# Performance work log

Measured on AMD Instinct MI355X. Metric: run time of the kernel, lower is better.

## Reference

```python
import jax, jax.numpy as jnp
import numpy as np

B, S, D, H = 4, 2048, 1024, 16
DK = D // H
NEG = -1e9


def setup_inputs() -> dict:
    key = jax.random.key(0)
    ks = jax.random.split(key, 8)
    q = jax.random.normal(ks[0], (B, S, D), dtype=jnp.float32)
    k = jax.random.normal(ks[1], (B, S, D), dtype=jnp.float32)
    v = jax.random.normal(ks[2], (B, S, D), dtype=jnp.float32)
    # causal mask, broadcastable to [B,H,S,S]; mask==0 -> masked out
    mask = jnp.tril(jnp.ones((S, S), dtype=jnp.int32))[None, None, :, :]
    scale = 1.0 / np.sqrt(D)
    w_q = jax.random.normal(ks[3], (D, D), dtype=jnp.float32) * scale
    w_k = jax.random.normal(ks[4], (D, D), dtype=jnp.float32) * scale
    w_v = jax.random.normal(ks[5], (D, D), dtype=jnp.float32) * scale
    w_o = jax.random.normal(ks[6], (D, D), dtype=jnp.float32) * scale
    return {"q": q, "k": k, "v": v, "mask": mask,
            "w_q": w_q, "w_k": w_k, "w_v": w_v, "w_o": w_o}


def reference(q, k, v, mask, w_q, w_k, w_v, w_o):
    # projections (nn.Linear with no bias: x @ W^T)
    def proj(x, w):
        y = jnp.einsum('bsd,ed->bse', x, w)          # [B,S,D]
        return y.reshape(B, -1, H, DK).transpose(0, 2, 1, 3)  # [B,H,S,DK]
    Q, K, V = proj(q, w_q), proj(k, w_k), proj(v, w_v)
    scores = jnp.einsum('bhqd,bhkd->bhqk', Q, K) * (DK ** -0.5)  # [B,H,S,S]
    scores = jnp.where(mask == 0, NEG, scores)
    attn = jax.nn.softmax(scores, axis=-1)
    x = jnp.einsum('bhqk,bhkd->bhqd', attn, V)       # [B,H,S,DK]
    x = x.transpose(0, 2, 1, 3).reshape(B, -1, D)    # [B,S,D]
    return jnp.einsum('bsd,ed->bse', x, w_o)
```

## Files before the change

### kernel.cpp

```cpp
#include <hip/hip_runtime.h>
#include <hip/hip_bf16.h>
#include <stdint.h>

#define B_ 4
#define S_ 2048
#define D_ 1024
#define H_ 16
#define DK_ 64

typedef __hip_bfloat16 bf16;
typedef __attribute__((ext_vector_type(8))) __bf16 bf16x8;
typedef __attribute__((ext_vector_type(4))) __bf16 bf16x4;
typedef __attribute__((ext_vector_type(4))) float f32x4;
typedef __attribute__((ext_vector_type(4))) uint32_t u32x4;

#define QSCALE 0.18033688011112042f

#if defined(__has_builtin)
#if __has_builtin(__builtin_amdgcn_exp2f)
#define EXP2(x) __builtin_amdgcn_exp2f(x)
#endif
#endif
#ifndef EXP2
#define EXP2(x) exp2f(x)
#endif

__device__ __forceinline__ void async_copy16(const void* g, void* l) {
    __builtin_amdgcn_global_load_lds((const __attribute__((address_space(1))) void*)g,
                                     (__attribute__((address_space(3))) void*)l,
                                     16, 0, 0);
}

__device__ __forceinline__ bf16x8 ld8(const bf16* p) {
    return *(const bf16x8*)p;
}

__device__ __forceinline__ uint32_t pk2(float a, float b) {
    union { __bf16 h; uint16_t u; } x, y;
    x.h = (__bf16)a; y.h = (__bf16)b;
    return (uint32_t)x.u | ((uint32_t)y.u << 16);
}

__device__ __forceinline__ bf16x8 cvt8(float4 u0, float4 u1) {
    return (bf16x8){(__bf16)u0.x, (__bf16)u0.y, (__bf16)u0.z, (__bf16)u0.w,
                    (__bf16)u1.x, (__bf16)u1.y, (__bf16)u1.z, (__bf16)u1.w};
}

__device__ __forceinline__ bf16x8 transpose_p(const float* p0, const float* p1,
                                              int srcl, bool loT) {
    uint32_t x0 = pk2(p0[0], p0[1]), x1 = pk2(p0[2], p0[3]);
    uint32_t y0 = pk2(p1[0], p1[1]), y1 = pk2(p1[2], p1[3]);
    u32x4 dw;
#pragma unroll
    for (int i = 0; i < 4; i++) {
        int sl = srcl + (i >> 1) * 16;
        uint32_t vA = (uint32_t)__shfl((int)((i & 1) ? x1 : x0), sl, 64);
        uint32_t vB = (uint32_t)__shfl((int)((i & 1) ? y1 : y0), sl, 64);
        dw[i] = loT ? vA : vB;
    }
    return __builtin_bit_cast(bf16x8, dw);
}

__global__ __launch_bounds__(256) void cvtw(const float4* __restrict__ s0,
                                            const float4* __restrict__ s1,
                                            const float4* __restrict__ s2,
                                            const float4* __restrict__ s3,
                                            bf16x4* __restrict__ d0,
                                            bf16x4* __restrict__ d1,
                                            bf16x4* __restrict__ d2,
                                            bf16x4* __restrict__ d3) {
    int i = blockIdx.x * 256 + threadIdx.x;
    int seg = i >> 18;
    int j   = i & 262143;
    const float4* s = seg == 0 ? s0 : seg == 1 ? s1 : seg == 2 ? s2 : s3;
    bf16x4*       d = seg == 0 ? d0 : seg == 1 ? d1 : seg == 2 ? d2 : d3;
    float4 f = s[j];
    d[j] = (bf16x4){(__bf16)f.x, (__bf16)f.y, (__bf16)f.z, (__bf16)f.w};
}

__global__ __launch_bounds__(256) void cvtx(const float* __restrict__ s0,
                                            const float* __restrict__ s1,
                                            const float* __restrict__ s2,
                                            bf16* __restrict__ d0,
                                            bf16* __restrict__ d1,
                                            bf16* __restrict__ d2) {
    const int z = blockIdx.z;
    const float* s = z == 0 ? s0 : z == 1 ? s1 : s2;
    bf16*        d = z == 0 ? d0 : z == 1 ? d1 : d2;
    size_t i = ((size_t)blockIdx.x * 256 + threadIdx.x) * 8;
    float4 u0 = *(const float4*)(s + i);
    float4 u1 = *(const float4*)(s + i + 4);
    *(bf16x8*)(d + i) = cvt8(u0, u1);
}

__global__ __launch_bounds__(256) void gemm_qkv_bf(const bf16* __restrict__ Aq,
                                                   const bf16* __restrict__ Ak,
                                                   const bf16* __restrict__ Av,
                                                   const bf16* __restrict__ Wqb,
                                                   const bf16* __restrict__ Wkb,
                                                   const bf16* __restrict__ Wvb,
                                                   bf16* __restrict__ Oq,
                                                   bf16* __restrict__ Ok,
                                                   bf16* __restrict__ Ov) {
    __shared__ bf16 lA[128 * 32];
    __shared__ bf16 lW[128 * 32];
    const int z = blockIdx.z;
    const bf16* A = z == 0 ? Aq : z == 1 ? Ak : Av;
    const bf16* W = z == 0 ? Wqb : z == 1 ? Wkb : Wvb;
    bf16*      out = z == 0 ? Oq : z == 1 ? Ok : Ov;

    const int tid  = threadIdx.x;
    const int lane = tid & 63;
    const int quad = lane >> 4;
    const int lo   = lane & 15;
    const int wave = tid >> 6;
    const int wm   = (wave >> 1) * 64;
    const int wn   = (wave & 1) * 64;
    const int n0   = blockIdx.x * 128;
    const int m0   = blockIdx.y * 128;
    const int K    = 1024;

    f32x4 acc[4][4];
#pragma unroll
    for (int i = 0; i < 4; i++)
#pragma unroll
        for (int j = 0; j < 4; j++) acc[i][j] = (f32x4){0.f, 0.f, 0.f, 0.f};

    const int sr = tid >> 2;
    const int sc = (tid & 3) * 8;

    for (int k0 = 0; k0 < K; k0 += 32) {
        async_copy16(A + (size_t)(m0 + sr) * K + k0 + sc,       lA + sr * 32 + sc);
        async_copy16(A + (size_t)(m0 + 64 + sr) * K + k0 + sc,  lA + (64 + sr) * 32 + sc);
        async_copy16(W + (size_t)(n0 + sr) * K + k0 + sc,       lW + sr * 32 + sc);
        async_copy16(W + (size_t)(n0 + 64 + sr) * K + k0 + sc,  lW + (64 + sr) * 32 + sc);
        __syncthreads();

        bf16x8 af[4], bfr[4];
#pragma unroll
        for (int i = 0; i < 4; i++)
            af[i] = ld8(lA + (wm + i * 16 + lo) * 32 + quad * 8);
#pragma unroll
        for (int j = 0; j < 4; j++)
            bfr[j] = ld8(lW + (wn + j * 16 + lo) * 32 + quad * 8);
#pragma unroll
        for (int i = 0; i < 4; i++)
#pragma unroll
            for (int j = 0; j < 4; j++)
                acc[i][j] = __builtin_amdgcn_mfma_f32_16x16x32_bf16(af[i], bfr[j], acc[i][j], 0, 0, 0);
        __syncthreads();
    }

#pragma unroll
    for (int i = 0; i < 4; i++)
#pragma unroll
        for (int j = 0; j < 4; j++)
#pragma unroll
            for (int r = 0; r < 4; r++) {
                int m = m0 + wm + i * 16 + quad * 4 + r;
                int n = n0 + wn + j * 16 + lo;
                float val = acc[i][j][r];
                int b = m >> 11, s = m & (S_ - 1);
                int h = n >> 6, dk = n & 63;
                if (z == 0) {
                    out[((size_t)(b * H_ + h) * S_ + s) * DK_ + dk] =
                        __float2bfloat16(val * QSCALE);
                } else if (z == 1) {
                    out[((size_t)(b * H_ + h) * S_ + s) * DK_ + dk] = __float2bfloat16(val);
                } else {
                    out[((size_t)(b * H_ + h) * DK_ + dk) * S_ + s] = __float2bfloat16(val);
                }
            }
}

__global__ __launch_bounds__(256) void gemm_qkv(const float* __restrict__ Aq,
                                                const float* __restrict__ Ak,
                                                const float* __restrict__ Av,
                                                const bf16* __restrict__ Wqb,
                                                const bf16* __restrict__ Wkb,
                                                const bf16* __restrict__ Wvb,
                                                bf16* __restrict__ Oq,
                                                bf16* __restrict__ Ok,
                                                bf16* __restrict__ Ov) {
    __shared__ bf16 lA[128 * 32];
    __shared__ bf16 lW[128 * 32];
    const int z = blockIdx.z;
    const float* A = z == 0 ? Aq : z == 1 ? Ak : Av;
    const bf16*  W = z == 0 ? Wqb : z == 1 ? Wkb : Wvb;
    bf16*      out = z == 0 ? Oq : z == 1 ? Ok : Ov;

    const int tid  = threadIdx.x;
    const int lane = tid & 63;
    const int quad = lane >> 4;
    const int lo   = lane & 15;
    const int wave = tid >> 6;
    const int wm   = (wave >> 1) * 64;
    const int wn   = (wave & 1) * 64;
    const int n0   = blockIdx.x * 128;
    const int m0   = blockIdx.y * 128;
    const int K    = 1024;

    f32x4 acc[4][4];
#pragma unroll
    for (int i = 0; i < 4; i++)
#pragma unroll
        for (int j = 0; j < 4; j++) acc[i][j] = (f32x4){0.f, 0.f, 0.f, 0.f};

    const int sr = tid >> 2;
    const int sc = (tid & 3) * 8;

    for (int k0 = 0; k0 < K; k0 += 32) {
        async_copy16(W + (size_t)(n0 + sr) * K + k0 + sc,       lW + sr * 32 + sc);
        async_copy16(W + (size_t)(n0 + 64 + sr) * K + k0 + sc,  lW + (64 + sr) * 32 + sc);
        const float* a0 = A + (size_t)(m0 + sr) * K + k0 + sc;
        const float* a1 = A + (size_t)(m0 + 64 + sr) * K + k0 + sc;
        float4 u0 = *(const float4*)a0;
        float4 u1 = *(const float4*)(a0 + 4);
        float4 u2 = *(const float4*)a1;
        float4 u3 = *(const float4*)(a1 + 4);
        *(bf16x8*)(lA + sr * 32 + sc)        = cvt8(u0, u1);
        *(bf16x8*)(lA + (64 + sr) * 32 + sc) = cvt8(u2, u3);
        __syncthreads();

        bf16x8 af[4], bfr[4];
#pragma unroll
        for (int i = 0; i < 4; i++)
            af[i] = ld8(lA + (wm + i * 16 + lo) * 32 + quad * 8);
#pragma unroll
        for (int j = 0; j < 4; j++)
            bfr[j] = ld8(lW + (wn + j * 16 + lo) * 32 + quad * 8);
#pragma unroll
        for (int i = 0; i < 4; i++)
#pragma unroll
            for (int j = 0; j < 4; j++)
                acc[i][j] = __builtin_amdgcn_mfma_f32_16x16x32_bf16(af[i], bfr[j], acc[i][j], 0, 0, 0);
        __syncthreads();
    }

#pragma unroll
    for (int i = 0; i < 4; i++)
#pragma unroll
        for (int j = 0; j < 4; j++)
#pragma unroll
            for (int r = 0; r < 4; r++) {
                int m = m0 + wm + i * 16 + quad * 4 + r;
                int n = n0 + wn + j * 16 + lo;
                float val = acc[i][j][r];
                int b = m >> 11, s = m & (S_ - 1);
                int h = n >> 6, dk = n & 63;
                if (z == 0) {
                    out[((size_t)(b * H_ + h) * S_ + s) * DK_ + dk] =
                        __float2bfloat16(val * QSCALE);
                } else if (z == 1) {
                    out[((size_t)(b * H_ + h) * S_ + s) * DK_ + dk] = __float2bfloat16(val);
                } else {
                    out[((size_t)(b * H_ + h) * DK_ + dk) * S_ + s] = __float2bfloat16(val);
                }
            }
}

__global__ __launch_bounds__(256) void gemm_out(const bf16* __restrict__ A,
                                                const bf16* __restrict__ W,
                                                float* __restrict__ out) {
    __shared__ bf16 lA[128 * 32];
    __shared__ bf16 lW[128 * 32];
    const int tid  = threadIdx.x;
    const int lane = tid & 63;
    const int quad = lane >> 4;
    const int lo   = lane & 15;
    const int wave = tid >> 6;
    const int wm   = (wave >> 1) * 64;
    const int wn   = (wave & 1) * 64;
    const int n0   = blockIdx.x * 128;
    const int m0   = blockIdx.y * 128;
    const int K    = 1024;

    f32x4 acc[4][4];
#pragma unroll
    for (int i = 0; i < 4; i++)
#pragma unroll
        for (int j = 0; j < 4; j++) acc[i][j] = (f32x4){0.f, 0.f, 0.f, 0.f};

    const int sr = tid >> 2;
    const int sc = (tid & 3) * 8;

    for (int k0 = 0; k0 < K; k0 += 32) {
        async_copy16(A + (size_t)(m0 + sr) * K + k0 + sc,       lA + sr * 32 + sc);
        async_copy16(A + (size_t)(m0 + 64 + sr) * K + k0 + sc,  lA + (64 + sr) * 32 + sc);
        async_copy16(W + (size_t)(n0 + sr) * K + k0 + sc,       lW + sr * 32 + sc);
        async_copy16(W + (size_t)(n0 + 64 + sr) * K + k0 + sc,  lW + (64 + sr) * 32 + sc);
        __syncthreads();

        bf16x8 af[4], bfr[4];
#pragma unroll
        for (int i = 0; i < 4; i++)
            af[i] = ld8(lA + (wm + i * 16 + lo) * 32 + quad * 8);
#pragma unroll
        for (int j = 0; j < 4; j++)
            bfr[j] = ld8(lW + (wn + j * 16 + lo) * 32 + quad * 8);
#pragma unroll
        for (int i = 0; i < 4; i++)
#pragma unroll
            for (int j = 0; j < 4; j++)
                acc[i][j] = __builtin_amdgcn_mfma_f32_16x16x32_bf16(af[i], bfr[j], acc[i][j], 0, 0, 0);
        __syncthreads();
    }

#pragma unroll
    for (int i = 0; i < 4; i++)
#pragma unroll
        for (int j = 0; j < 4; j++)
#pragma unroll
            for (int r = 0; r < 4; r++) {
                int m = m0 + wm + i * 16 + quad * 4 + r;
                int n = n0 + wn + j * 16 + lo;
                out[(size_t)m * D_ + n] = acc[i][j][r];
            }
}

__global__ __launch_bounds__(64) void attn(const bf16* __restrict__ Q,
                                           const bf16* __restrict__ K,
                                           const bf16* __restrict__ Vt,
                                           bf16* __restrict__ X) {
    const int lane = threadIdx.x;
    const int quad = lane >> 4;
    const int lo   = lane & 15;
    const int idx  = blockIdx.x;
    const int bh   = idx & 63;
    const int qbp  = 31 - (idx >> 6);
    const int q0   = qbp * 64;

    const bf16* Qp = Q  + (size_t)bh * S_ * DK_;
    const bf16* Kp = K  + (size_t)bh * S_ * DK_;
    const bf16* Vp = Vt + (size_t)bh * DK_ * S_;

    bf16x8 bQ[4][2];
#pragma unroll
    for (int qs = 0; qs < 4; qs++) {
        const bf16* qp = Qp + (size_t)(q0 + qs * 16 + lo) * DK_ + quad * 8;
        bQ[qs][0] = ld8(qp);
        bQ[qs][1] = ld8(qp + 32);
    }

    f32x4 out[4][4];
    float lsum[4] = {0.f, 0.f, 0.f, 0.f};
#pragma unroll
    for (int qs = 0; qs < 4; qs++)
#pragma unroll
        for (int t = 0; t < 4; t++) out[qs][t] = (f32x4){0.f, 0.f, 0.f, 0.f};

    const int NT   = 2 * qbp + 2;
    const int srcl = (quad & 1) * 32 + lo;
    const bool loT = (quad < 2);

    bf16x8 aK0, aK1, aK2, aK3;
    {
        const bf16* kn = Kp + (size_t)lo * DK_ + quad * 8;
        aK0 = ld8(kn); aK1 = ld8(kn + 32);
        aK2 = ld8(kn + 16 * DK_); aK3 = ld8(kn + 16 * DK_ + 32);
    }

    for (int it = 0; it < NT; ++it) {
        const int kv0 = it * 32;
        const int am = (it < 2 * qbp) ? 0 : (it == 2 * qbp ? 1 : 2);
        const int bm = (it < 2 * qbp + 1) ? 0 : 1;

        bf16x8 aV[4];
#pragma unroll
        for (int t = 0; t < 4; t++)
            aV[t] = ld8(Vp + (size_t)(t * 16 + lo) * S_ + kv0 + quad * 8);

        f32x4 st[4][2];
        __builtin_amdgcn_s_setprio(1);
#pragma unroll
        for (int qs = 0; qs < 4; qs++) {
            f32x4 t0 = (f32x4){0.f, 0.f, 0.f, 0.f};
            f32x4 t1 = (f32x4){0.f, 0.f, 0.f, 0.f};
            t0 = __builtin_amdgcn_mfma_f32_16x16x32_bf16(aK0, bQ[qs][0], t0, 0, 0, 0);
            t0 = __builtin_amdgcn_mfma_f32_16x16x32_bf16(aK1, bQ[qs][1], t0, 0, 0, 0);
            t1 = __builtin_amdgcn_mfma_f32_16x16x32_bf16(aK2, bQ[qs][0], t1, 0, 0, 0);
            t1 = __builtin_amdgcn_mfma_f32_16x16x32_bf16(aK3, bQ[qs][1], t1, 0, 0, 0);
            st[qs][0] = t0; st[qs][1] = t1;
        }
        __builtin_amdgcn_s_setprio(0);

        {
            int kvn = it + 1; if (kvn >= NT) kvn = NT - 1;
            const bf16* kn = Kp + (size_t)(kvn * 32 + lo) * DK_ + quad * 8;
            aK0 = ld8(kn); aK1 = ld8(kn + 32);
            aK2 = ld8(kn + 16 * DK_); aK3 = ld8(kn + 16 * DK_ + 32);
        }

        bf16x8 bP[4];
#pragma unroll
        for (int pr = 0; pr < 2; pr++) {
            const int mode = pr == 0 ? am : bm;
            const int sl = pr * 2, sh = pr * 2 + 1;
            float pl0[4], pl1[4], ph0[4], ph1[4];
#pragma unroll
            for (int r = 0; r < 4; r++) {
                float el0 = EXP2(st[sl][0][r]);
                float el1 = EXP2(st[sl][1][r]);
                float eh0 = EXP2(st[sh][0][r]);
                float eh1 = EXP2(st[sh][1][r]);
                if (mode == 1) {
                    bool c = (quad * 4 + r) <= lo;
                    el0 = c ? el0 : 0.f;
                    el1 = 0.f;
                    eh1 = c ? eh1 : 0.f;
                } else if (mode == 2) {
                    el0 = 0.f; el1 = 0.f; eh0 = 0.f; eh1 = 0.f;
                }
                pl0[r] = el0; pl1[r] = el1; ph0[r] = eh0; ph1[r] = eh1;
                lsum[sl] += el0 + el1;
                lsum[sh] += eh0 + eh1;
            }
            bP[sl] = transpose_p(pl0, pl1, srcl, loT);
            bP[sh] = transpose_p(ph0, ph1, srcl, loT);
        }

        __builtin_amdgcn_s_setprio(1);
#pragma unroll
        for (int qs = 0; qs < 4; qs++)
#pragma unroll
            for (int t = 0; t < 4; t++)
                out[qs][t] = __builtin_amdgcn_mfma_f32_16x16x32_bf16(aV[t], bP[qs], out[qs][t], 0, 0, 0);
        __builtin_amdgcn_s_setprio(0);
    }

    const int b = bh >> 4, h = bh & 15;
#pragma unroll
    for (int qs = 0; qs < 4; qs++) {
        float ls = lsum[qs];
        ls += __shfl_xor(ls, 16, 64);
        ls += __shfl_xor(ls, 32, 64);
        const float rl = 1.f / ls;
        bf16* Xp = X + (size_t)(b * S_ + q0 + qs * 16 + lo) * D_ + h * 64;
#pragma unroll
        for (int t = 0; t < 4; t++) {
            uint32_t* d = (uint32_t*)(Xp + t * 16 + quad * 4);
            d[0] = pk2(out[qs][t][0] * rl, out[qs][t][1] * rl);
            d[1] = pk2(out[qs][t][2] * rl, out[qs][t][3] * rl);
        }
    }
}

extern "C" void kernel_launch(void* const* d_in, const int* in_sizes, int n_in,
                              void* d_out, int out_size, void* d_ws, size_t ws_size,
                              hipStream_t stream) {
    const float* q  = (const float*)d_in[0];
    const float* k  = (const float*)d_in[1];
    const float* v  = (const float*)d_in[2];
    const float* wq = (const float*)d_in[4];
    const float* wk = (const float*)d_in[5];
    const float* wv = (const float*)d_in[6];
    const float* wo = (const float*)d_in[7];

    const size_t elems  = (size_t)B_ * S_ * D_;
    const size_t welems = (size_t)D_ * D_;
    bf16* WoB = (bf16*)d_ws;
    bf16* WqB = WoB + welems;
    bf16* WkB = WqB + welems;
    bf16* WvB = WkB + welems;
    bf16* Xb  = WqB;
    bf16* Qw  = WqB + elems;
    bf16* Kw  = Qw + elems;
    bf16* Vw  = Kw + elems;
    bf16* Aqb = Vw + elems;
    bf16* Akb = Aqb + elems;
    bf16* Avb = Akb + elems;

    const size_t need_big = ((size_t)(Avb + elems) - (size_t)d_ws);

    hipLaunchKernelGGL(cvtw, dim3(4 * (int)(welems / 4) / 256), dim3(256), 0, stream,
                       (const float4*)wq, (const float4*)wk, (const float4*)wv,
                       (const float4*)wo,
                       (bf16x4*)WqB, (bf16x4*)WkB, (bf16x4*)WvB, (bf16x4*)WoB);

    if (ws_size >= need_big) {
        hipLaunchKernelGGL(cvtx, dim3((int)(elems / 8 / 256), 1, 3), dim3(256), 0, stream,
                           q, k, v, Aqb, Akb, Avb);
        hipLaunchKernelGGL(gemm_qkv_bf, dim3(D_ / 128, (B_ * S_) / 128, 3), dim3(256), 0,
                           stream, Aqb, Akb, Avb, WqB, WkB, WvB, Qw, Kw, Vw);
    } else {
        hipLaunchKernelGGL(gemm_qkv, dim3(D_ / 128, (B_ * S_) / 128, 3), dim3(256), 0,
                           stream, q, k, v, WqB, WkB, WvB, Qw, Kw, Vw);
    }

    hipLaunchKernelGGL(attn, dim3((S_ / 64) * B_ * H_), dim3(64), 0, stream, Qw, Kw, Vw, Xb);
    hipLaunchKernelGGL(gemm_out, dim3(D_ / 128, (B_ * S_) / 128), dim3(256), 0, stream,
                       Xb, WoB, (float*)d_out);
}
```

Before: 372.8 us.

## Split attention KV loop across two waves with LDS reduction

Each attention block now runs two wavefronts, and each wave processes half of the KV tiles for the same 64-query block. Wave 1 writes its partial output accumulators and row sums to shared memory, and wave 0 merges them before normalizing and storing. This works without max-rescaling because the softmax uses unnormalized exp2 with no running max. The aim is to halve the serial per-block KV loop and raise parallelism. The cost is LDS traffic, a block barrier, and an idle wave 1 during the epilogue.

```diff
diff --git a/kernel.cpp b/kernel.cpp
--- a/kernel.cpp
+++ b/kernel.cpp
@@ -318,11 +318,15 @@
             }
 }
 
-__global__ __launch_bounds__(64) void attn(const bf16* __restrict__ Q,
-                                           const bf16* __restrict__ K,
-                                           const bf16* __restrict__ Vt,
-                                           bf16* __restrict__ X) {
-    const int lane = threadIdx.x;
+__global__ __launch_bounds__(128) void attn(const bf16* __restrict__ Q,
+                                            const bf16* __restrict__ K,
+                                            const bf16* __restrict__ Vt,
+                                            bf16* __restrict__ X) {
+    __shared__ f32x4 sO[4][4][64];
+    __shared__ float sL[4][64];
+    const int tid  = threadIdx.x;
+    const int wid  = tid >> 6;
+    const int lane = tid & 63;
     const int quad = lane >> 4;
     const int lo   = lane & 15;
     const int idx  = blockIdx.x;
@@ -350,17 +354,20 @@
         for (int t = 0; t < 4; t++) out[qs][t] = (f32x4){0.f, 0.f, 0.f, 0.f};
 
     const int NT   = 2 * qbp + 2;
+    const int half = NT >> 1;
+    const int it0  = wid * half;
+    const int it1  = it0 + half;
     const int srcl = (quad & 1) * 32 + lo;
     const bool loT = (quad < 2);
 
     bf16x8 aK0, aK1, aK2, aK3;
     {
-        const bf16* kn = Kp + (size_t)lo * DK_ + quad * 8;
+        const bf16* kn = Kp + (size_t)(it0 * 32 + lo) * DK_ + quad * 8;
         aK0 = ld8(kn); aK1 = ld8(kn + 32);
         aK2 = ld8(kn + 16 * DK_); aK3 = ld8(kn + 16 * DK_ + 32);
     }
 
-    for (int it = 0; it < NT; ++it) {
+    for (int it = it0; it < it1; ++it) {
         const int kv0 = it * 32;
         const int am = (it < 2 * qbp) ? 0 : (it == 2 * qbp ? 1 : 2);
         const int bm = (it < 2 * qbp + 1) ? 0 : 1;
@@ -385,7 +392,7 @@
         __builtin_amdgcn_s_setprio(0);
 
         {
-            int kvn = it + 1; if (kvn >= NT) kvn = NT - 1;
+            int kvn = it + 1; if (kvn >= it1) kvn = it1 - 1;
             const bf16* kn = Kp + (size_t)(kvn * 32 + lo) * DK_ + quad * 8;
             aK0 = ld8(kn); aK1 = ld8(kn + 32);
             aK2 = ld8(kn + 16 * DK_); aK3 = ld8(kn + 16 * DK_ + 32);
@@ -428,19 +435,36 @@
         __builtin_amdgcn_s_setprio(0);
     }
 
-    const int b = bh >> 4, h = bh & 15;
-#pragma unroll
-    for (int qs = 0; qs < 4; qs++) {
-        float ls = lsum[qs];
-        ls += __shfl_xor(ls, 16, 64);
-        ls += __shfl_xor(ls, 32, 64);
-        const float rl = 1.f / ls;
-        bf16* Xp = X + (size_t)(b * S_ + q0 + qs * 16 + lo) * D_ + h * 64;
-#pragma unroll
-        for (int t = 0; t < 4; t++) {
-            uint32_t* d = (uint32_t*)(Xp + t * 16 + quad * 4);
-            d[0] = pk2(out[qs][t][0] * rl, out[qs][t][1] * rl);
-            d[1] = pk2(out[qs][t][2] * rl, out[qs][t][3] * rl);
+    if (wid == 1) {
+#pragma unroll
+        for (int qs = 0; qs < 4; qs++) {
+#pragma unroll
+            for (int t = 0; t < 4; t++) sO[qs][t][lane] = out[qs][t];
+            sL[qs][lane] = lsum[qs];
+        }
+    }
+    __syncthreads();
+    if (wid == 0) {
+        const int b = bh >> 4, h = bh & 15;
+#pragma unroll
+        for (int qs = 0; qs < 4; qs++) {
+#pragma unroll
+            for (int t = 0; t < 4; t++) {
+                f32x4 p = sO[qs][t][lane];
+                out[qs][t][0] += p[0]; out[qs][t][1] += p[1];
+                out[qs][t][2] += p[2]; out[qs][t][3] += p[3];
+            }
+            float ls = lsum[qs] + sL[qs][lane];
+            ls += __shfl_xor(ls, 16, 64);
+            ls += __shfl_xor(ls, 32, 64);
+            const float rl = 1.f / ls;
+            bf16* Xp = X + (size_t)(b * S_ + q0 + qs * 16 + lo) * D_ + h * 64;
+#pragma unroll
+            for (int t = 0; t < 4; t++) {
+                uint32_t* d = (uint32_t*)(Xp + t * 16 + quad * 4);
+                d[0] = pk2(out[qs][t][0] * rl, out[qs][t][1] * rl);
+                d[1] = pk2(out[qs][t][2] * rl, out[qs][t][3] * rl);
+            }
         }
     }
 }
@@ -487,7 +511,7 @@
                            stream, q, k, v, WqB, WkB, WvB, Qw, Kw, Vw);
     }
 
-    hipLaunchKernelGGL(attn, dim3((S_ / 64) * B_ * H_), dim3(64), 0, stream, Qw, Kw, Vw, Xb);
+    hipLaunchKernelGGL(attn, dim3((S_ / 64) * B_ * H_), dim3(128), 0, stream, Qw, Kw, Vw, Xb);
     hipLaunchKernelGGL(gemm_out, dim3(D_ / 128, (B_ * S_) / 128), dim3(256), 0, stream,
                        Xb, WoB, (float*)d_out);
 }
```

Measured after the change: 358.3 us. 1.04x faster.
